# Optimization experiments

Measured on AMD Instinct MI355X. Metric: run time of the kernel, lower is better.

Reference implementation:

```python
import jax, jax.numpy as jnp
import numpy as np

D_MODEL = 768
N_HEADS = 12
D_HEAD = D_MODEL // N_HEADS
D_FF = 3072
B, T = 2, 4096
EPS = 1e-5


def _layer_norm(x, gamma, beta):
    mu = jnp.mean(x, axis=-1, keepdims=True)
    var = jnp.var(x, axis=-1, keepdims=True)
    return (x - mu) * jax.lax.rsqrt(var + EPS) * gamma + beta


def setup_inputs() -> dict:
    key = jax.random.key(0)
    ks = jax.random.split(key, 20)
    s = 0.02
    def lin(k, din, dout):
        return jax.random.normal(k, (din, dout), jnp.float32) * s
    inp = {
        "x": jax.random.normal(ks[0], (B, T, D_MODEL), jnp.float32),
        "wq": lin(ks[1], D_MODEL, D_MODEL), "bq": jnp.zeros((D_MODEL,), jnp.float32),
        "wk": lin(ks[2], D_MODEL, D_MODEL), "bk": jnp.zeros((D_MODEL,), jnp.float32),
        "wv": lin(ks[3], D_MODEL, D_MODEL), "bv": jnp.zeros((D_MODEL,), jnp.float32),
        "wo": lin(ks[4], D_MODEL, D_MODEL), "bo": jnp.zeros((D_MODEL,), jnp.float32),
        "w1": lin(ks[5], D_MODEL, D_FF), "b1": jnp.zeros((D_FF,), jnp.float32),
        "w2": lin(ks[6], D_FF, D_MODEL), "b2": jnp.zeros((D_MODEL,), jnp.float32),
        "g1": jnp.ones((D_MODEL,), jnp.float32), "be1": jnp.zeros((D_MODEL,), jnp.float32),
        "g2": jnp.ones((D_MODEL,), jnp.float32), "be2": jnp.zeros((D_MODEL,), jnp.float32),
    }
    return inp


def reference(x, wq, bq, wk, bk, wv, bv, wo, bo, w1, b1, w2, b2, g1, be1, g2, be2):
    Bx, Tx, D = x.shape
    # --- multi-head causal self-attention (naive, full TxT scores) ---
    def split_heads(t):
        return t.reshape(Bx, Tx, N_HEADS, D_HEAD).transpose(0, 2, 1, 3)  # [B,H,T,dh]
    Q = split_heads(x @ wq + bq)
    K = split_heads(x @ wk + bk)
    V = split_heads(x @ wv + bv)
    scores = jnp.einsum("bhqd,bhkd->bhqk", Q, K) / (D_HEAD ** 0.5)
    causal = jnp.tril(jnp.ones((Tx, Tx), bool))
    scores = jnp.where(causal, scores, -jnp.inf)
    weights = jax.nn.softmax(scores, axis=-1)
    attn = jnp.einsum("bhqk,bhkd->bhqd", weights, V)
    attn = attn.transpose(0, 2, 1, 3).reshape(Bx, Tx, D)
    attn_out = attn @ wo + bo
    # --- residual + LN1 ---
    h = _layer_norm(x + attn_out, g1, be1)
    # --- FFN ---
    ffn = jax.nn.relu(h @ w1 + b1) @ w2 + b2
    # --- residual + LN2 ---
    return _layer_norm(h + ffn, g2, be2)
```

## Files before the change

kernel.cpp:

```cpp
#include <hip/hip_runtime.h>
#include <hip/hip_bf16.h>

typedef __hip_bfloat16 bf16;
typedef __attribute__((ext_vector_type(8))) short short8;
typedef __attribute__((ext_vector_type(4))) short short4b;
typedef __attribute__((ext_vector_type(4))) float floatx4;

#define DM   768
#define NH   12
#define DH   64
#define DFF  3072
#define TS   4096
#define NB   2
#define MTOK (NB * TS)
#define EPS  1e-5f
#define NEG  -30000.0f

__device__ __forceinline__ float b2f(bf16 v)  { return __bfloat162float(v); }
__device__ __forceinline__ bf16  f2b(float v) { return __float2bfloat16(v); }
__device__ __forceinline__ short sbf(float x) { bf16 b = __float2bfloat16(x); return *(short*)&b; }
__device__ __forceinline__ float ldf(const float* p) { return *p; }
__device__ __forceinline__ float ldf(const bf16*  p) { return b2f(*p); }
__device__ __forceinline__ void stf(float* p, float v) { *p = v; }
__device__ __forceinline__ void stf(bf16*  p, float v) { *p = f2b(v); }

__device__ __forceinline__ void gl2lds(const bf16* g, short* l) {
    __builtin_amdgcn_global_load_lds(
        (const __attribute__((address_space(1))) void*)g,
        (__attribute__((address_space(3))) void*)l, 16, 0, 0);
}

template <int RELU>
__global__ __launch_bounds__(256)
void gemm_lds(const bf16* __restrict__ A, int lda, const bf16* __restrict__ Wt,
              const float* __restrict__ bias, bf16* __restrict__ C, int ldc,
              int N, int K)
{
    __shared__ __align__(16) short As[2][128 * 32];
    __shared__ __align__(16) short Bs[2][128 * 32];

    const int tid  = threadIdx.x;
    const int wave = tid >> 6, lane = tid & 63;
    const int wx = wave & 1, wy = wave >> 1;
    const int quad = lane >> 4, fn = lane & 15;
    const int bm = blockIdx.y * 128, bn = blockIdx.x * 128;
    const int l4 = lane >> 2, l8 = (lane & 3) * 8;

    const bf16* gA0 = A  + (size_t)(bm + wave * 16       + l4) * lda + l8;
    const bf16* gA1 = A  + (size_t)(bm + (wave + 4) * 16 + l4) * lda + l8;
    const bf16* gB0 = Wt + (size_t)(bn + wave * 16       + l4) * K   + l8;
    const bf16* gB1 = Wt + (size_t)(bn + (wave + 4) * 16 + l4) * K   + l8;
    const int cA0 = wave * 512, cA1 = (wave + 4) * 512;

    floatx4 acc[4][4] = {};

    for (int kk = 0; kk < K; kk += 64) {
        __syncthreads();
        gl2lds(gA0 + kk,      &As[0][cA0]);
        gl2lds(gA1 + kk,      &As[0][cA1]);
        gl2lds(gB0 + kk,      &Bs[0][cA0]);
        gl2lds(gB1 + kk,      &Bs[0][cA1]);
        gl2lds(gA0 + kk + 32, &As[1][cA0]);
        gl2lds(gA1 + kk + 32, &As[1][cA1]);
        gl2lds(gB0 + kk + 32, &Bs[1][cA0]);
        gl2lds(gB1 + kk + 32, &Bs[1][cA1]);
        __syncthreads();

        #pragma unroll
        for (int h = 0; h < 2; ++h) {
            short8 af[4], bfr[4];
            #pragma unroll
            for (int i = 0; i < 4; ++i) {
                af[i]  = *(const short8*)&As[h][(wy * 64 + i * 16 + fn) * 32 + quad * 8];
                bfr[i] = *(const short8*)&Bs[h][(wx * 64 + i * 16 + fn) * 32 + quad * 8];
            }
            #pragma unroll
            for (int i = 0; i < 4; ++i)
                #pragma unroll
                for (int j = 0; j < 4; ++j)
                    acc[i][j] = __builtin_amdgcn_mfma_f32_16x16x32_bf16(
                        af[i], bfr[j], acc[i][j], 0, 0, 0);
        }
    }

    #pragma unroll
    for (int j = 0; j < 4; ++j) {
        const int n = bn + wx * 64 + j * 16 + fn;
        const float bv = bias[n];
        #pragma unroll
        for (int i = 0; i < 4; ++i) {
            #pragma unroll
            for (int rg = 0; rg < 4; ++rg) {
                const int m = bm + wy * 64 + i * 16 + quad * 4 + rg;
                float v = acc[i][j][rg] + bv;
                if (RELU) v = fmaxf(v, 0.f);
                C[(size_t)m * ldc + n] = f2b(v);
            }
        }
    }
}

template <int RELU>
__global__ __launch_bounds__(256)
void gemm_lds64(const bf16* __restrict__ A, int lda, const bf16* __restrict__ Wt,
                const float* __restrict__ bias, bf16* __restrict__ C, int ldc,
                int N, int K)
{
    __shared__ __align__(16) short As[2][64 * 32];
    __shared__ __align__(16) short Bs[2][64 * 32];

    const int tid  = threadIdx.x;
    const int wave = tid >> 6, lane = tid & 63;
    const int wx = wave & 1, wy = wave >> 1;
    const int quad = lane >> 4, fn = lane & 15;
    const int bm = blockIdx.y * 64, bn = blockIdx.x * 64;
    const int l4 = lane >> 2, l8 = (lane & 3) * 8;

    const bf16* gA = A  + (size_t)(bm + wave * 16 + l4) * lda + l8;
    const bf16* gB = Wt + (size_t)(bn + wave * 16 + l4) * K   + l8;
    const int cw = wave * 512;

    floatx4 acc[2][2] = {};

    for (int kk = 0; kk < K; kk += 64) {
        __syncthreads();
        gl2lds(gA + kk,      &As[0][cw]);
        gl2lds(gB + kk,      &Bs[0][cw]);
        gl2lds(gA + kk + 32, &As[1][cw]);
        gl2lds(gB + kk + 32, &Bs[1][cw]);
        __syncthreads();

        #pragma unroll
        for (int h = 0; h < 2; ++h) {
            short8 af[2], bfr[2];
            #pragma unroll
            for (int i = 0; i < 2; ++i) {
                af[i]  = *(const short8*)&As[h][(wy * 32 + i * 16 + fn) * 32 + quad * 8];
                bfr[i] = *(const short8*)&Bs[h][(wx * 32 + i * 16 + fn) * 32 + quad * 8];
            }
            #pragma unroll
            for (int i = 0; i < 2; ++i)
                #pragma unroll
                for (int j = 0; j < 2; ++j)
                    acc[i][j] = __builtin_amdgcn_mfma_f32_16x16x32_bf16(
                        af[i], bfr[j], acc[i][j], 0, 0, 0);
        }
    }

    #pragma unroll
    for (int j = 0; j < 2; ++j) {
        const int n = bn + wx * 32 + j * 16 + fn;
        const float bv = bias[n];
        #pragma unroll
        for (int i = 0; i < 2; ++i) {
            #pragma unroll
            for (int rg = 0; rg < 4; ++rg) {
                const int m = bm + wy * 32 + i * 16 + quad * 4 + rg;
                float v = acc[i][j][rg] + bv;
                if (RELU) v = fmaxf(v, 0.f);
                C[(size_t)m * ldc + n] = f2b(v);
            }
        }
    }
}

__global__ __launch_bounds__(256)
void xcvt(const float* __restrict__ x, bf16* __restrict__ xb)
{
    const size_t i = ((size_t)blockIdx.x * 256 + threadIdx.x) * 8;
    const float4 a = *(const float4*)&x[i];
    const float4 b = *(const float4*)&x[i + 4];
    short8 v;
    v[0]=sbf(a.x); v[1]=sbf(a.y); v[2]=sbf(a.z); v[3]=sbf(a.w);
    v[4]=sbf(b.x); v[5]=sbf(b.y); v[6]=sbf(b.z); v[7]=sbf(b.w);
    *(short8*)&xb[i] = v;
}

__global__ __launch_bounds__(256)
void attn_v9(const bf16* __restrict__ QKV, bf16* __restrict__ Out)
{
    __shared__ __align__(16) short Ks[64 * 72];
    __shared__ __align__(16) short Vt[64 * 72];
    __shared__ __align__(16) float Ss[4][16 * 68];
    __shared__ __align__(16) short Ps[4][16 * 72];
    __shared__ float Al[4][16];
    __shared__ float Ll[4][16];

    const int tid  = threadIdx.x;
    const int wave = tid >> 6, lane = tid & 63;
    const int quad = lane >> 4, fn = lane & 15;
    const int bh = blockIdx.y;
    const int b = bh / NH, h = bh % NH;
    const int bx = blockIdx.x;

    const int orow = lane >> 2;
    const int okey = (lane & 3) * 16;

    const short* QKVs = (const short*)QKV;

    const int sk = tid >> 3, sc8 = (tid & 7) * 8;
    const int vd = tid & 63, vk4 = (tid >> 6) * 4;
    const size_t gK = (size_t)(b * TS) * 2304 + 768  + h * 64 + (size_t)sk * 2304 + sc8;
    const size_t gV = (size_t)(b * TS) * 2304 + 1536 + h * 64 + vd;

    auto run = [&](const int q0) {
        const int nt = q0 / 64 + 1;
        const int qwmin = q0 + wave * 16;

        const size_t rowQ = (size_t)(b * TS + q0 + wave * 16 + fn) * 2304 + h * 64;
        const short8 qa0 = *(const short8*)&QKV[rowQ + quad * 8];
        const short8 qa1 = *(const short8*)&QKV[rowQ + 32 + quad * 8];

        float mrow = NEG, lrow = 0.f;
        floatx4 o[4] = {};

        short8 kr0 = *(const short8*)&QKVs[gK];
        short8 kr1 = *(const short8*)&QKVs[gK + (size_t)32 * 2304];
        short4b vr0, vr1, vr2, vr3;
        #pragma unroll
        for (int j = 0; j < 4; ++j) {
            vr0[j] = QKVs[gV + (size_t)(vk4 + j) * 2304];
            vr1[j] = QKVs[gV + (size_t)(16 + vk4 + j) * 2304];
            vr2[j] = QKVs[gV + (size_t)(32 + vk4 + j) * 2304];
            vr3[j] = QKVs[gV + (size_t)(48 + vk4 + j) * 2304];
        }

        for (int t = 0; t < nt; ++t) {
            const int kk0 = t * 64;
            __syncthreads();
            *(short8*)&Ks[sk * 72 + sc8]        = kr0;
            *(short8*)&Ks[(sk + 32) * 72 + sc8] = kr1;
            *(short4b*)&Vt[vd * 72 + vk4]       = vr0;
            *(short4b*)&Vt[vd * 72 + 16 + vk4]  = vr1;
            *(short4b*)&Vt[vd * 72 + 32 + vk4]  = vr2;
            *(short4b*)&Vt[vd * 72 + 48 + vk4]  = vr3;
            if (t + 1 < nt) {
                const size_t nk = (size_t)(kk0 + 64) * 2304;
                kr0 = *(const short8*)&QKVs[gK + nk];
                kr1 = *(const short8*)&QKVs[gK + nk + (size_t)32 * 2304];
                #pragma unroll
                for (int j = 0; j < 4; ++j) {
                    vr0[j] = QKVs[gV + nk + (size_t)(vk4 + j) * 2304];
                    vr1[j] = QKVs[gV + nk + (size_t)(16 + vk4 + j) * 2304];
                    vr2[j] = QKVs[gV + nk + (size_t)(32 + vk4 + j) * 2304];
                    vr3[j] = QKVs[gV + nk + (size_t)(48 + vk4 + j) * 2304];
                }
            }
            __syncthreads();

            if (kk0 > qwmin + 15) continue;

            __builtin_amdgcn_s_setprio(1);
            floatx4 s[4] = {};
            #pragma unroll
            for (int ks = 0; ks < 4; ++ks) {
                const short8 ka = *(const short8*)&Ks[(ks * 16 + fn) * 72 + quad * 8];
                const short8 kb = *(const short8*)&Ks[(ks * 16 + fn) * 72 + 32 + quad * 8];
                s[ks] = __builtin_amdgcn_mfma_f32_16x16x32_bf16(qa0, ka, s[ks], 0, 0, 0);
                s[ks] = __builtin_amdgcn_mfma_f32_16x16x32_bf16(qa1, kb, s[ks], 0, 0, 0);
            }
            __builtin_amdgcn_s_setprio(0);

            const int qg = q0 + wave * 16 + quad * 4;
            if (kk0 + 63 <= qwmin) {
                #pragma unroll
                for (int ks = 0; ks < 4; ++ks)
                    #pragma unroll
                    for (int rg = 0; rg < 4; ++rg)
                        Ss[wave][(quad * 4 + rg) * 68 + ks * 16 + fn] = s[ks][rg] * 0.125f;
            } else {
                #pragma unroll
                for (int ks = 0; ks < 4; ++ks)
                    #pragma unroll
                    for (int rg = 0; rg < 4; ++rg) {
                        const float v = (kk0 + ks * 16 + fn <= qg + rg)
                                            ? s[ks][rg] * 0.125f : NEG;
                        Ss[wave][(quad * 4 + rg) * 68 + ks * 16 + fn] = v;
                    }
            }

            float sv[16];
            *(float4*)&sv[0]  = *(const float4*)&Ss[wave][orow * 68 + okey];
            *(float4*)&sv[4]  = *(const float4*)&Ss[wave][orow * 68 + okey + 4];
            *(float4*)&sv[8]  = *(const float4*)&Ss[wave][orow * 68 + okey + 8];
            *(float4*)&sv[12] = *(const float4*)&Ss[wave][orow * 68 + okey + 12];
            float mx = sv[0];
            #pragma unroll
            for (int j = 1; j < 16; ++j) mx = fmaxf(mx, sv[j]);
            mx = fmaxf(mx, __shfl_xor(mx, 1, 64));
            mx = fmaxf(mx, __shfl_xor(mx, 2, 64));
            const float mn2 = fmaxf(mrow, mx);
            float ps = 0.f;
            short8 pb0, pb1;
            #pragma unroll
            for (int j = 0; j < 8; ++j) {
                const float p = __expf(fminf(sv[j] - mn2, 0.f));
                ps += p;
                pb0[j] = sbf(p);
            }
            #pragma unroll
            for (int j = 0; j < 8; ++j) {
                const float p = __expf(fminf(sv[8 + j] - mn2, 0.f));
                ps += p;
                pb1[j] = sbf(p);
            }
            ps += __shfl_xor(ps, 1, 64);
            ps += __shfl_xor(ps, 2, 64);
            const float cr = __expf(fminf(mrow - mn2, 0.f));
            lrow = lrow * cr + ps;
            mrow = mn2;
            *(short8*)&Ps[wave][orow * 72 + okey]     = pb0;
            *(short8*)&Ps[wave][orow * 72 + okey + 8] = pb1;
            if ((lane & 3) == 0) { Al[wave][orow] = cr; Ll[wave][orow] = lrow; }

            float al[4];
            #pragma unroll
            for (int rg = 0; rg < 4; ++rg) al[rg] = Al[wave][quad * 4 + rg];
            #pragma unroll
            for (int cb = 0; cb < 4; ++cb)
                #pragma unroll
                for (int rg = 0; rg < 4; ++rg) o[cb][rg] *= al[rg];
            const short8 pf0 = *(const short8*)&Ps[wave][fn * 72 + quad * 8];
            const short8 pf1 = *(const short8*)&Ps[wave][fn * 72 + 32 + quad * 8];
            __builtin_amdgcn_s_setprio(1);
            #pragma unroll
            for (int cb = 0; cb < 4; ++cb) {
                const short8 vfa = *(const short8*)&Vt[(cb * 16 + fn) * 72 + quad * 8];
                o[cb] = __builtin_amdgcn_mfma_f32_16x16x32_bf16(pf0, vfa, o[cb], 0, 0, 0);
            }
            #pragma unroll
            for (int cb = 0; cb < 4; ++cb) {
                const short8 vfb = *(const short8*)&Vt[(cb * 16 + fn) * 72 + 32 + quad * 8];
                o[cb] = __builtin_amdgcn_mfma_f32_16x16x32_bf16(pf1, vfb, o[cb], 0, 0, 0);
            }
            __builtin_amdgcn_s_setprio(0);
        }

        float li[4];
        #pragma unroll
        for (int rg = 0; rg < 4; ++rg)
            li[rg] = 1.f / fmaxf(Ll[wave][quad * 4 + rg], 1e-20f);
        #pragma unroll
        for (int cb = 0; cb < 4; ++cb)
            #pragma unroll
            for (int rg = 0; rg < 4; ++rg) {
                const size_t row = (size_t)(b * TS + q0 + wave * 16 + quad * 4 + rg);
                Out[row * DM + h * 64 + cb * 16 + fn] = f2b(o[cb][rg] * li[rg]);
            }
    };

    run((TS / 64 - 1 - bx) * 64);
    run(bx * 64);
}

__global__ __launch_bounds__(256)
void transW(const float* __restrict__ W, bf16* __restrict__ Wt, int K, int N)
{
    __shared__ float t[32][33];
    const int k0 = blockIdx.x * 32, n0 = blockIdx.y * 32;
    const int tx = threadIdx.x, ty = threadIdx.y;
    #pragma unroll
    for (int i = 0; i < 4; ++i)
        t[ty + i * 8][tx] = W[(size_t)(k0 + ty + i * 8) * N + n0 + tx];
    __syncthreads();
    #pragma unroll
    for (int i = 0; i < 4; ++i)
        Wt[(size_t)(n0 + ty + i * 8) * K + k0 + tx] = f2b(t[tx][ty + i * 8]);
}

__global__ __launch_bounds__(256)
void pack_bias(const float* __restrict__ bq, const float* __restrict__ bk,
               const float* __restrict__ bv, float* __restrict__ out)
{
    const int i = blockIdx.x * 256 + threadIdx.x;
    if (i < 3 * DM)
        out[i] = (i < DM) ? bq[i] : (i < 2 * DM) ? bk[i - DM] : bv[i - 2 * DM];
}

template <typename T1, typename T2, typename TOUT>
__global__ __launch_bounds__(256)
void add_ln(const T1* __restrict__ a, const T2* __restrict__ r, int ldr,
            const float* __restrict__ gamma, const float* __restrict__ beta,
            TOUT* __restrict__ out)
{
    const int row = blockIdx.x;
    const size_t offa = (size_t)row * DM;
    const size_t offr = (size_t)row * ldr;
    const int tid = threadIdx.x;

    float v[3];
    float s = 0.f, s2 = 0.f;
    #pragma unroll
    for (int j = 0; j < 3; ++j) {
        const int i = tid + j * 256;
        const float t = ldf(a + offa + i) + ldf(r + offr + i);
        v[j] = t; s += t; s2 += t * t;
    }
    __shared__ float red[256], red2[256];
    red[tid] = s; red2[tid] = s2;
    __syncthreads();
    #pragma unroll
    for (int st = 128; st > 0; st >>= 1) {
        if (tid < st) { red[tid] += red[tid + st]; red2[tid] += red2[tid + st]; }
        __syncthreads();
    }
    const float mu   = red[0] * (1.f / DM);
    const float var  = red2[0] * (1.f / DM) - mu * mu;
    const float rstd = rsqrtf(var + EPS);
    #pragma unroll
    for (int j = 0; j < 3; ++j) {
        const int i = tid + j * 256;
        stf(out + offa + i, (v[j] - mu) * rstd * gamma[i] + beta[i]);
    }
}

extern "C" void kernel_launch(void* const* d_in, const int* in_sizes, int n_in,
                              void* d_out, int out_size, void* d_ws, size_t ws_size,
                              hipStream_t stream)
{
    (void)in_sizes; (void)n_in; (void)out_size; (void)ws_size;

    const float* x   = (const float*)d_in[0];
    const float* wq  = (const float*)d_in[1];  const float* bq  = (const float*)d_in[2];
    const float* wk  = (const float*)d_in[3];  const float* bk  = (const float*)d_in[4];
    const float* wv  = (const float*)d_in[5];  const float* bv  = (const float*)d_in[6];
    const float* wo  = (const float*)d_in[7];  const float* bo  = (const float*)d_in[8];
    const float* w1  = (const float*)d_in[9];  const float* b1  = (const float*)d_in[10];
    const float* w2  = (const float*)d_in[11]; const float* b2  = (const float*)d_in[12];
    const float* g1  = (const float*)d_in[13]; const float* be1 = (const float*)d_in[14];
    const float* g2  = (const float*)d_in[15]; const float* be2 = (const float*)d_in[16];

    const size_t S = (size_t)MTOK * DM;
    bf16* QKVb = (bf16*)d_ws;
    bf16* Hb   = QKVb + 3 * S;
    bf16* wbuf = Hb + S;
    float* bqkv = (float*)(wbuf + (size_t)2 * DFF * DM);
    bf16* F1 = QKVb;
    bf16* Yb = QKVb + 2 * S;
    bf16* Pb = QKVb + DM;
    bf16* Ao = Hb;
    bf16* xb = Hb;

    const dim3 tblk(32, 8);
    const dim3 blk(256);

    xcvt<<<dim3(3072), blk, 0, stream>>>(x, xb);

    transW<<<dim3(24, 24), tblk, 0, stream>>>(wq, wbuf,                    DM, DM);
    transW<<<dim3(24, 24), tblk, 0, stream>>>(wk, wbuf + (size_t)DM * DM,  DM, DM);
    transW<<<dim3(24, 24), tblk, 0, stream>>>(wv, wbuf + (size_t)2*DM*DM,  DM, DM);
    pack_bias<<<dim3(9), blk, 0, stream>>>(bq, bk, bv, bqkv);
    gemm_lds<0><<<dim3(18, 64), blk, 0, stream>>>(
        xb, DM, wbuf, bqkv, QKVb, 3 * DM, 3 * DM, DM);

    attn_v9<<<dim3(32, NB * NH), blk, 0, stream>>>(QKVb, Ao);

    transW<<<dim3(24, 24), tblk, 0, stream>>>(wo, wbuf, DM, DM);
    gemm_lds64<0><<<dim3(12, 128), blk, 0, stream>>>(
        Ao, DM, wbuf, bo, Pb, 3 * DM, DM, DM);
    add_ln<float, bf16, bf16><<<dim3(MTOK), blk, 0, stream>>>(
        x, Pb, 3 * DM, g1, be1, Hb);

    transW<<<dim3(24, 96), tblk, 0, stream>>>(w1, wbuf, DM, DFF);
    bf16* w2t = wbuf + (size_t)DFF * DM;
    transW<<<dim3(96, 24), tblk, 0, stream>>>(w2, w2t, DFF, DM);
    for (int m0 = 0; m0 < MTOK; m0 += 4096) {
        gemm_lds<1><<<dim3(24, 32), blk, 0, stream>>>(
            Hb + (size_t)m0 * DM, DM, wbuf, b1, F1, DFF, DFF, DM);
        gemm_lds64<0><<<dim3(12, 64), blk, 0, stream>>>(
            F1, DFF, w2t, b2, Yb + (size_t)m0 * DM, DM, DM, DFF);
    }

    add_ln<bf16, bf16, float><<<dim3(MTOK), blk, 0, stream>>>(
        Hb, Yb, DM, g2, be2, (float*)d_out);
}
```

Baseline: 551.6 us.

## Swizzle block IDs across XCDs and use exp2 softmax in attention

Remaps linear block IDs so that consecutive logical tiles land on the same XCD, applied to both GEMM kernels and the attention kernel, with the aim of improving L2 reuse of shared A/B tiles and K/V rows. The attention softmax now folds log2(e) into the score scale and uses exp2f without the fminf clamp, removing a multiply and a min per exponent. The swizzle assumes the block count is divisible by 8, and the exp2 change relies on scores staying at or below the running max.

After: 616.9 us. 1.12x slower.

```diff
diff --git a/kernel.cpp b/kernel.cpp
--- a/kernel.cpp
+++ b/kernel.cpp
@@ -15,6 +15,7 @@
 #define MTOK (NB * TS)
 #define EPS  1e-5f
 #define NEG  -30000.0f
+#define SCL2 0.18033688f
 
 __device__ __forceinline__ float b2f(bf16 v)  { return __bfloat162float(v); }
 __device__ __forceinline__ bf16  f2b(float v) { return __float2bfloat16(v); }
@@ -30,6 +31,10 @@
         (__attribute__((address_space(3))) void*)l, 16, 0, 0);
 }
 
+__device__ __forceinline__ int xcd_swz(int lid, int nblk) {
+    return (lid & 7) * (nblk >> 3) + (lid >> 3);
+}
+
 template <int RELU>
 __global__ __launch_bounds__(256)
 void gemm_lds(const bf16* __restrict__ A, int lda, const bf16* __restrict__ Wt,
@@ -43,7 +48,14 @@
     const int wave = tid >> 6, lane = tid & 63;
     const int wx = wave & 1, wy = wave >> 1;
     const int quad = lane >> 4, fn = lane & 15;
-    const int bm = blockIdx.y * 128, bn = blockIdx.x * 128;
+
+    const int nb  = gridDim.x * gridDim.y;
+    const int lid = blockIdx.y * gridDim.x + blockIdx.x;
+    const int w   = xcd_swz(lid, nb);
+    const int bxw = w / gridDim.y;
+    const int byw = w % gridDim.y;
+    const int bm = byw * 128, bn = bxw * 128;
+
     const int l4 = lane >> 2, l8 = (lane & 3) * 8;
 
     const bf16* gA0 = A  + (size_t)(bm + wave * 16       + l4) * lda + l8;
@@ -113,7 +125,14 @@
     const int wave = tid >> 6, lane = tid & 63;
     const int wx = wave & 1, wy = wave >> 1;
     const int quad = lane >> 4, fn = lane & 15;
-    const int bm = blockIdx.y * 64, bn = blockIdx.x * 64;
+
+    const int nb  = gridDim.x * gridDim.y;
+    const int lid = blockIdx.y * gridDim.x + blockIdx.x;
+    const int w   = xcd_swz(lid, nb);
+    const int bxw = w / gridDim.y;
+    const int byw = w % gridDim.y;
+    const int bm = byw * 64, bn = bxw * 64;
+
     const int l4 = lane >> 2, l8 = (lane & 3) * 8;
 
     const bf16* gA = A  + (size_t)(bm + wave * 16 + l4) * lda + l8;
@@ -177,7 +196,7 @@
 }
 
 __global__ __launch_bounds__(256)
-void attn_v9(const bf16* __restrict__ QKV, bf16* __restrict__ Out)
+void attn_v10(const bf16* __restrict__ QKV, bf16* __restrict__ Out)
 {
     __shared__ __align__(16) short Ks[64 * 72];
     __shared__ __align__(16) short Vt[64 * 72];
@@ -189,9 +208,12 @@
     const int tid  = threadIdx.x;
     const int wave = tid >> 6, lane = tid & 63;
     const int quad = lane >> 4, fn = lane & 15;
-    const int bh = blockIdx.y;
+
+    const int lid = blockIdx.y * gridDim.x + blockIdx.x;
+    const int w   = xcd_swz(lid, gridDim.x * gridDim.y);
+    const int bh  = w >> 5;
+    const int bx  = w & 31;
     const int b = bh / NH, h = bh % NH;
-    const int bx = blockIdx.x;
 
     const int orow = lane >> 2;
     const int okey = (lane & 3) * 16;
@@ -267,14 +289,14 @@
                 for (int ks = 0; ks < 4; ++ks)
                     #pragma unroll
                     for (int rg = 0; rg < 4; ++rg)
-                        Ss[wave][(quad * 4 + rg) * 68 + ks * 16 + fn] = s[ks][rg] * 0.125f;
+                        Ss[wave][(quad * 4 + rg) * 68 + ks * 16 + fn] = s[ks][rg] * SCL2;
             } else {
                 #pragma unroll
                 for (int ks = 0; ks < 4; ++ks)
                     #pragma unroll
                     for (int rg = 0; rg < 4; ++rg) {
                         const float v = (kk0 + ks * 16 + fn <= qg + rg)
-                                            ? s[ks][rg] * 0.125f : NEG;
+                                            ? s[ks][rg] * SCL2 : NEG;
                         Ss[wave][(quad * 4 + rg) * 68 + ks * 16 + fn] = v;
                     }
             }
@@ -294,19 +316,19 @@
             short8 pb0, pb1;
             #pragma unroll
             for (int j = 0; j < 8; ++j) {
-                const float p = __expf(fminf(sv[j] - mn2, 0.f));
+                const float p = exp2f(sv[j] - mn2);
                 ps += p;
                 pb0[j] = sbf(p);
             }
             #pragma unroll
             for (int j = 0; j < 8; ++j) {
-                const float p = __expf(fminf(sv[8 + j] - mn2, 0.f));
+                const float p = exp2f(sv[8 + j] - mn2);
                 ps += p;
                 pb1[j] = sbf(p);
             }
             ps += __shfl_xor(ps, 1, 64);
             ps += __shfl_xor(ps, 2, 64);
-            const float cr = __expf(fminf(mrow - mn2, 0.f));
+            const float cr = exp2f(mrow - mn2);
             lrow = lrow * cr + ps;
             mrow = mn2;
             *(short8*)&Ps[wave][orow * 72 + okey]     = pb0;
@@ -453,7 +475,7 @@
     gemm_lds<0><<<dim3(18, 64), blk, 0, stream>>>(
         xb, DM, wbuf, bqkv, QKVb, 3 * DM, 3 * DM, DM);
 
-    attn_v9<<<dim3(32, NB * NH), blk, 0, stream>>>(QKVb, Ao);
+    attn_v10<<<dim3(32, NB * NH), blk, 0, stream>>>(QKVb, Ao);
 
     transW<<<dim3(24, 24), tblk, 0, stream>>>(wo, wbuf, DM, DM);
     gemm_lds64<0><<<dim3(12, 128), blk, 0, stream>>>(
```
